# Optimization experiments

Hardware: AMD Instinct MI355X
Metric: run time of the kernel (lower is better)

The kernel has to match this reference:

```python
import jax, jax.numpy as jnp
from jax import lax
import numpy as np

B, T, H, K = 32, 512, 2048, 128


def setup_inputs() -> dict:
    key = jax.random.key(0)
    k1, k2, k3, k4, k5, k6, k7 = jax.random.split(key, 7)
    hiddens = jax.random.normal(k1, (B, T, H), dtype=jnp.float32)
    mask = jnp.ones((B, T), dtype=jnp.int32)  # mask[:,0] must be on (torchcrf)
    labels = jax.random.randint(k2, (B, T), 0, K)
    W = jax.random.normal(k3, (H, K), dtype=jnp.float32) * 0.02
    b = jnp.zeros((K,), dtype=jnp.float32)
    # torchcrf inits transitions uniform(-0.1, 0.1)
    start_transitions = jax.random.uniform(k4, (K,), minval=-0.1, maxval=0.1)
    end_transitions = jax.random.uniform(k5, (K,), minval=-0.1, maxval=0.1)
    transitions = jax.random.uniform(k6, (K, K), minval=-0.1, maxval=0.1)
    return {"hiddens": hiddens, "mask": mask, "labels": labels, "W": W, "b": b,
            "start_transitions": start_transitions, "end_transitions": end_transitions,
            "transitions": transitions}


def _crf_log_likelihood(emissions, tags, mask, start_t, end_t, trans):
    # emissions: [B,T,K], tags/mask: [B,T]
    Bn, Tn, Kn = emissions.shape
    maskf = mask.astype(emissions.dtype)
    # ---- numerator: score of the gold path ----
    score = start_t[tags[:, 0]] + emissions[jnp.arange(Bn), 0, tags[:, 0]]
    prev, cur = tags[:, :-1], tags[:, 1:]
    emit_cur = jnp.take_along_axis(emissions[:, 1:], cur[..., None], axis=-1)[..., 0]
    score = score + jnp.sum((trans[prev, cur] + emit_cur) * maskf[:, 1:], axis=1)
    last_idx = mask.sum(axis=1).astype(jnp.int32) - 1
    last_tags = jnp.take_along_axis(tags, last_idx[:, None], axis=1)[:, 0]
    score = score + end_t[last_tags]
    # ---- denominator: log partition via stable logsumexp scan ----
    def step(alpha, inp):
        emit_t, m_t = inp  # [B,K], [B]
        nxt = jax.nn.logsumexp(alpha[:, :, None] + trans[None] + emit_t[:, None, :], axis=1)
        alpha = jnp.where(m_t[:, None] > 0, nxt, alpha)
        return alpha, None
    alpha0 = start_t[None, :] + emissions[:, 0]
    emits = jnp.swapaxes(emissions[:, 1:], 0, 1)  # [T-1,B,K]
    ms = jnp.swapaxes(mask[:, 1:], 0, 1)          # [T-1,B]
    alpha, _ = lax.scan(step, alpha0, (emits, ms))
    logZ = jax.nn.logsumexp(alpha + end_t[None, :], axis=1)
    return score - logZ


def _viterbi_decode(emissions, mask, start_t, end_t, trans):
    Bn, Tn, Kn = emissions.shape
    tag_ids = jnp.arange(Kn, dtype=jnp.int32)
    def step(score, inp):
        emit_t, m_t = inp
        cand = score[:, :, None] + trans[None]          # [B,K,K] prev->cur
        bp = jnp.argmax(cand, axis=1).astype(jnp.int32)  # [B,K]
        best = jnp.max(cand, axis=1) + emit_t
        on = m_t[:, None] > 0
        new_score = jnp.where(on, best, score)
        bp = jnp.where(on, bp, tag_ids[None, :])  # identity for padded steps
        return new_score, bp
    score0 = start_t[None, :] + emissions[:, 0]
    emits = jnp.swapaxes(emissions[:, 1:], 0, 1)
    ms = jnp.swapaxes(mask[:, 1:], 0, 1)
    score, history = lax.scan(step, score0, (emits, ms))  # history: [T-1,B,K]
    last_tag = jnp.argmax(score + end_t[None, :], axis=1).astype(jnp.int32)  # [B]
    def back(tag, bp_t):
        tag = jnp.take_along_axis(bp_t, tag[:, None], axis=1)[:, 0]
        return tag, tag
    _, tags_prev = lax.scan(back, last_tag, history, reverse=True)  # [T-1,B]
    tags = jnp.concatenate([tags_prev, last_tag[None, :]], axis=0)  # [T,B]
    return jnp.swapaxes(tags, 0, 1)  # [B,T]


def reference(hiddens, mask, labels, W, b, start_transitions, end_transitions, transitions):
    logits = jnp.einsum('bth,hk->btk', hiddens, W) + b  # emission projection
    decode = _viterbi_decode(logits, mask, start_transitions, end_transitions, transitions)
    llh = _crf_log_likelihood(logits, labels, mask, start_transitions, end_transitions, transitions)
    loss = -jnp.mean(llh)  # -1 * crf(..., reduction='mean')
    return (decode, loss)
```

## Files before the change

### kernel.cpp

```cpp
#include <hip/hip_runtime.h>
#include <hip/hip_bf16.h>
#include <math.h>

#define BB 32
#define TT 512
#define HH 2048
#define KK 128

__global__ __launch_bounds__(512) void gemm_k(const float* __restrict__ hid,
                                              const float* __restrict__ Wm,
                                              const float* __restrict__ bias,
                                              float* __restrict__ logits,
                                              float* __restrict__ loss_slot) {
    __shared__ union {
        struct { float As[4][16][72]; float Bs[4][16][132]; } s;
        float4 red[16][128];
    } sm;
    const int tid = threadIdx.x, bid = blockIdx.x;
    if (bid == 0 && tid == 0) loss_slot[0] = 0.0f;
    const int g = tid >> 7, lt = tid & 127;
    const int rowBase = bid * 64;
    const int rowg = lt >> 4, colg = lt & 15;
    const int arow = lt >> 1, ahq = lt & 1;

    float acc[8][8];
#pragma unroll
    for (int i = 0; i < 8; i++)
#pragma unroll
        for (int j = 0; j < 8; j++) acc[i][j] = 0.0f;

    const float* hA = hid + (size_t)(rowBase + arow) * HH + g * 512 + ahq * 8;

    float4 a0, a1, bv[4];
    {
        const int h0 = g * 512;
        a0 = *(const float4*)(hA);
        a1 = *(const float4*)(hA + 4);
#pragma unroll
        for (int r = 0; r < 4; ++r) {
            int idx = r * 128 + lt;
// ... 47 lines not shown
        if (g == gp) {
#pragma unroll
            for (int i = 0; i < 8; ++i) {
                sm.red[i * 2][lt] = make_float4(acc[i][0], acc[i][1], acc[i][2], acc[i][3]);
                sm.red[i * 2 + 1][lt] = make_float4(acc[i][4], acc[i][5], acc[i][6], acc[i][7]);
            }
        }
        __syncthreads();
        if (g == 0) {
#pragma unroll
            for (int i = 0; i < 8; ++i) {
                float4 r0 = sm.red[i * 2][lt];
                float4 r1 = sm.red[i * 2 + 1][lt];
                acc[i][0] += r0.x; acc[i][1] += r0.y; acc[i][2] += r0.z; acc[i][3] += r0.w;
                acc[i][4] += r1.x; acc[i][5] += r1.y; acc[i][6] += r1.z; acc[i][7] += r1.w;
            }
        }
        __syncthreads();
    }
    if (g == 0) {
        float4 bb0 = *(const float4*)(bias + colg * 4);
        float4 bb1 = *(const float4*)(bias + 64 + colg * 4);
#pragma unroll
        for (int i = 0; i < 8; ++i) {
            int row = rowBase + rowg * 8 + i;
            *(float4*)(logits + (size_t)row * KK + colg * 4) =
                make_float4(acc[i][0] + bb0.x, acc[i][1] + bb0.y, acc[i][2] + bb0.z, acc[i][3] + bb0.w);
            *(float4*)(logits + (size_t)row * KK + 64 + colg * 4) =
                make_float4(acc[i][4] + bb1.x, acc[i][5] + bb1.y, acc[i][6] + bb1.z, acc[i][7] + bb1.w);
        }
    }
}

struct SMemB {
    float ubuf[2][144];
    float red[4];
    float vbuf[128];
};

__global__ __launch_bounds__(256) void scan_k(const float* __restrict__ logits,
                                              const int* __restrict__ mask,
                                              const int* __restrict__ labels,
                                              const float* __restrict__ startT,
                                              const float* __restrict__ endT,
                                              const float* __restrict__ trans,
                                              float* __restrict__ shist,
                                              float* __restrict__ out) {
    __shared__ SMemB sm;
    const int tid = threadIdx.x;
    const int bid = blockIdx.x;
    const float L2E = 1.4426950408889634f;
    const int s = tid & 3;
    const int jb = tid >> 2;
    const int j0 = jb * 2;
    const int padw = j0 + 4 * (j0 >> 5);
    const int lane = tid & 63;

    if (bid < BB) {
        const int b = bid;
        const float* lrow = logits + (size_t)b * TT * KK;
        unsigned long long mb[8];
#pragma unroll
        for (int c = 0; c < 8; ++c) mb[c] = __ballot(mask[b * TT + c * 64 + lane]);
        float V0[32], V1[32];
#pragma unroll
        for (int k = 0; k < 32; k++) {
            V0[k] = exp2f(trans[(s * 32 + k) * KK + j0] * L2E);
            V1[k] = exp2f(trans[(s * 32 + k) * KK + j0 + 1] * L2E);
        }
        float a0_ = (startT[j0] + lrow[j0]) * L2E;
        float a1_ = (startT[j0 + 1] + lrow[j0 + 1]) * L2E;
        float OFF = (startT[0] + lrow[0]) * L2E;
        float S0_ = exp2f(a0_ - OFF);
        float S1_ = exp2f(a1_ - OFF);
        if (s == 0) {
            sm.ubuf[0][padw] = S0_;
            sm.ubuf[0][padw + 1] = S1_;
        }
        float2 emq[4];
#pragma unroll
        for (int d = 0; d < 4; ++d) emq[d] = *(const float2*)(lrow + (size_t)(1 + d) * KK + j0);
        float2 scc = make_float2(exp2f(emq[0].x * L2E), exp2f(emq[0].y * L2E));
        __syncthreads();
        int cur = 0;
        for (int t = 1; t < TT; ++t) {
            float2 sc = scc;
            emq[0] = emq[1]; emq[1] = emq[2]; emq[2] = emq[3];
            if (t + 4 < TT) emq[3] = *(const float2*)(lrow + (size_t)(t + 4) * KK + j0);
            scc = make_float2(exp2f(emq[0].x * L2E), exp2f(emq[0].y * L2E));
            int mt = (int)((mb[t >> 6] >> (t & 63)) & 1ull);
            if (mt) {
                const float* ub = &sm.ubuf[cur][s * 36];
                float u00 = sm.ubuf[cur][0];
                float uu[32];
#pragma unroll
                for (int c = 0; c < 8; ++c) {
                    float4 v = *(const float4*)(ub + c * 4);
                    uu[c * 4] = v.x; uu[c * 4 + 1] = v.y; uu[c * 4 + 2] = v.z; uu[c * 4 + 3] = v.w;
                }
                float r00 = __builtin_amdgcn_rcpf(u00);
                OFF += log2f(u00);
                float p0[4] = {0.f, 0.f, 0.f, 0.f}, p1[4] = {0.f, 0.f, 0.f, 0.f};
#pragma unroll
                for (int k = 0; k < 32; k += 4) {
#pragma unroll
                    for (int q = 0; q < 4; ++q) {
                        p0[q] = fmaf(uu[k + q], V0[k + q], p0[q]);
                        p1[q] = fmaf(uu[k + q], V1[k + q], p1[q]);
                    }
                }
                float w0 = (p0[0] + p0[1]) + (p0[2] + p0[3]);
                float w1 = (p1[0] + p1[1]) + (p1[2] + p1[3]);
                w0 += __shfl_xor(w0, 1, 64);
                w0 += __shfl_xor(w0, 2, 64);
                w1 += __shfl_xor(w1, 1, 64);
                w1 += __shfl_xor(w1, 2, 64);
                S0_ = w0 * (sc.x * r00);
                S1_ = w1 * (sc.y * r00);
                if (s == 0) {
                    sm.ubuf[cur ^ 1][padw] = S0_;
                    sm.ubuf[cur ^ 1][padw + 1] = S1_;
                }
                cur ^= 1;
            }
            __syncthreads();
        }
        if (s == 0) {
            sm.vbuf[j0] = log2f(S0_) + endT[j0] * L2E;
            sm.vbuf[j0 + 1] = log2f(S1_) + endT[j0 + 1] * L2E;
        }
        __syncthreads();

        float part = 0.0f;
        for (int tt = tid; tt < TT; tt += 256) {
            if (tt == 0) {
                int l0 = labels[b * TT];
                part += startT[l0] + lrow[l0];
            } else if (mask[b * TT + tt]) {
                int lc = labels[b * TT + tt];
                int lp = labels[b * TT + tt - 1];
                part += trans[lp * KK + lc] + lrow[(size_t)tt * KK + lc];
            }
        }
#pragma unroll
        for (int d = 1; d < 64; d <<= 1) part += __shfl_xor(part, d, 64);
        int wid = tid >> 6;
        if (lane == 0) sm.red[wid] = part;
        __syncthreads();
        if (tid < 64) {
            float v0 = sm.vbuf[tid], v1 = sm.vbuf[tid + 64];
            float mx = fmaxf(v0, v1);
#pragma unroll
            for (int d = 1; d < 64; d <<= 1) mx = fmaxf(mx, __shfl_xor(mx, d, 64));
            float p = exp2f(v0 - mx) + exp2f(v1 - mx);
#pragma unroll
            for (int d = 1; d < 64; d <<= 1) p += __shfl_xor(p, d, 64);
            if (tid == 0) {
                int total = 0;
#pragma unroll
                for (int c = 0; c < 8; ++c) total += __popcll(mb[c]);
                float score = sm.red[0] + sm.red[1] + sm.red[2] + sm.red[3];
                score += endT[labels[b * TT + total - 1]];
                float logZ = (OFF + mx + log2f(p)) * 0.6931471805599453f;
                float llh = score - logZ;
                atomicAdd(out + BB * TT, -llh * (1.0f / 32.0f));
            }
        }
    } else {
        const int b = bid - BB;
        const float* lrow = logits + (size_t)b * TT * KK;
        float* hist = shist + (size_t)b * TT * KK;
        unsigned long long mb[8];
#pragma unroll
        for (int c = 0; c < 8; ++c) mb[c] = __ballot(mask[b * TT + c * 64 + lane]);
        float T0[32], T1[32];
#pragma unroll
        for (int k = 0; k < 32; k++) {
            T0[k] = trans[(s * 32 + k) * KK + j0];
            T1[k] = trans[(s * 32 + k) * KK + j0 + 1];
        }
        float s0_ = startT[j0] + lrow[j0];
        float s1_ = startT[j0 + 1] + lrow[j0 + 1];
        if (s == 0) {
            sm.ubuf[0][padw] = s0_;
            sm.ubuf[0][padw + 1] = s1_;
        } else if (s == 1) {
            *(float2*)(hist + j0) = make_float2(s0_, s1_);
        }
        float2 emq[4];
#pragma unroll
        for (int d = 0; d < 4; ++d) emq[d] = *(const float2*)(lrow + (size_t)(1 + d) * KK + j0);
        __syncthreads();
        int cur = 0;
        for (int t = 1; t < TT; ++t) {
            float2 em = emq[0];
            emq[0] = emq[1]; emq[1] = emq[2]; emq[2] = emq[3];
            if (t + 4 < TT) emq[3] = *(const float2*)(lrow + (size_t)(t + 4) * KK + j0);
            int mt = (int)((mb[t >> 6] >> (t & 63)) & 1ull);
            if (mt) {
                const float* ub = &sm.ubuf[cur][s * 36];
                float uu[32];
#pragma unroll
                for (int c = 0; c < 8; ++c) {
                    float4 v = *(const float4*)(ub + c * 4);
                    uu[c * 4] = v.x; uu[c * 4 + 1] = v.y; uu[c * 4 + 2] = v.z; uu[c * 4 + 3] = v.w;
                }
                float m0a = -3.0e38f, m0b = -3.0e38f, m1a = -3.0e38f, m1b = -3.0e38f;
#pragma unroll
                for (int k = 0; k < 32; k += 4) {
                    m0a = fmaxf(m0a, fmaxf(uu[k] + T0[k], uu[k + 1] + T0[k + 1]));
                    m0b = fmaxf(m0b, fmaxf(uu[k + 2] + T0[k + 2], uu[k + 3] + T0[k + 3]));
                    m1a = fmaxf(m1a, fmaxf(uu[k] + T1[k], uu[k + 1] + T1[k + 1]));
                    m1b = fmaxf(m1b, fmaxf(uu[k + 2] + T1[k + 2], uu[k + 3] + T1[k + 3]));
                }
                float m0 = fmaxf(m0a, m0b), m1 = fmaxf(m1a, m1b);
                m0 = fmaxf(m0, __shfl_xor(m0, 1, 64));
                m0 = fmaxf(m0, __shfl_xor(m0, 2, 64));
                m1 = fmaxf(m1, __shfl_xor(m1, 1, 64));
                m1 = fmaxf(m1, __shfl_xor(m1, 2, 64));
                s0_ = m0 + em.x;
                s1_ = m1 + em.y;
                if (s == 0) {
                    sm.ubuf[cur ^ 1][padw] = s0_;
                    sm.ubuf[cur ^ 1][padw + 1] = s1_;
                } else if (s == 1) {
                    *(float2*)(hist + (size_t)t * KK + j0) = make_float2(s0_, s1_);
                }
                cur ^= 1;
            } else {
                if (s == 1) *(float2*)(hist + (size_t)t * KK + j0) = make_float2(s0_, s1_);
            }
            __syncthreads();
        }
    }
}

__global__ __launch_bounds__(256) void bp_k(const float* __restrict__ shist,
                                            const float* __restrict__ trans,
                                            const int* __restrict__ mask,
                                            unsigned char* __restrict__ bp) {
    const int t = blockIdx.x + 1;
    const int tid = threadIdx.x;
    const int j = tid & 127, bg = tid >> 7;
    __shared__ float sc[BB][KK];
#pragma unroll
    for (int r = 0; r < 4; ++r) {
        int f = tid + r * 256;
        int bb2 = f >> 5, c4 = (f & 31) * 4;
        *(float4*)&sc[bb2][c4] = *(const float4*)&shist[(size_t)bb2 * TT * KK + (size_t)(t - 1) * KK + c4];
    }
    __syncthreads();
    float m[16];
    int idx[16];
#pragma unroll
    for (int c = 0; c < 16; c++) { m[c] = -3.0e38f; idx[c] = 0; }
    for (int i4 = 0; i4 < 32; ++i4) {
        const int ib = i4 * 4;
        float tr0 = trans[(ib + 0) * KK + j];
        float tr1 = trans[(ib + 1) * KK + j];
        float tr2 = trans[(ib + 2) * KK + j];
        float tr3 = trans[(ib + 3) * KK + j];
#pragma unroll
        for (int c = 0; c < 16; c++) {
            float4 s4 = *(const float4*)&sc[bg + 2 * c][ib];
            float c0 = s4.x + tr0, c1 = s4.y + tr1, c2 = s4.z + tr2, c3 = s4.w + tr3;
// ... 50 lines not shown
                int t_row = ph * 64 + 1 + r;
                if (t_row < TT) {
                    unsigned int vv = (unsigned int)__shfl((int)reg[r], tag >> 1, 64);
                    tag = (int)((vv >> ((tag & 1) * 8)) & 0xffu);
                    if (lane == 0) tagbuf[t_row - 1] = tag;
                }
            }
            if (lane == 0) handoff = tag;
        }
        __syncthreads();
    }
    out[b * TT + tid] = (float)tagbuf[tid];
}

extern "C" void kernel_launch(void* const* d_in, const int* in_sizes, int n_in,
                              void* d_out, int out_size, void* d_ws, size_t ws_size,
                              hipStream_t stream) {
    const float* hid = (const float*)d_in[0];
    const int* mask = (const int*)d_in[1];
    const int* labels = (const int*)d_in[2];
    const float* Wm = (const float*)d_in[3];
    const float* bias = (const float*)d_in[4];
    const float* startT = (const float*)d_in[5];
    const float* endT = (const float*)d_in[6];
    const float* trans = (const float*)d_in[7];
    float* out = (float*)d_out;
    char* ws = (char*)d_ws;

    float* logits = (float*)ws;
    float* shist = (float*)(ws + 8388608);
    unsigned char* bp = (unsigned char*)(ws + 16777216);

    gemm_k<<<256, 512, 0, stream>>>(hid, Wm, bias, logits, out + BB * TT);
    scan_k<<<64, 256, 0, stream>>>(logits, mask, labels, startT, endT, trans, shist, out);
    bp_k<<<TT - 1, 256, 0, stream>>>(shist, trans, mask, bp);
    bt_k<<<BB, 512, 0, stream>>>(shist, endT, bp, out);
}
```

Measured before the change: 665.4 us.

## Stage emission logits in shared-memory chunks and batch Viterbi history stores

Both sequential scan loops now load emissions in chunks of 8 timesteps. Each thread issues one coalesced float4 load per chunk, and the data is double-buffered in LDS instead of each thread keeping a 4-deep register queue of strided float2 global loads. The Viterbi path also buffers its per-step score history in registers and writes all 8 steps to global memory at the end of each chunk, rather than storing every step. The aim is to take global-load latency and store traffic off the per-timestep critical path. The cost is more LDS, extra register pressure, and moving the exp2 of the emission back onto the serial dependency chain in the forward scan.

```diff
diff --git a/kernel.cpp b/kernel.cpp
--- a/kernel.cpp
+++ b/kernel.cpp
@@ -6,6 +6,7 @@
 #define TT 512
 #define HH 2048
 #define KK 128
+#define CH 8
 
 __global__ __launch_bounds__(512) void gemm_k(const float* __restrict__ hid,
                                               const float* __restrict__ Wm,
@@ -121,6 +122,7 @@
 
 struct SMemB {
     float ubuf[2][144];
+    float em[2][CH * KK];
     float red[4];
     float vbuf[128];
 };
@@ -142,6 +144,7 @@
     const int j0 = jb * 2;
     const int padw = j0 + 4 * (j0 >> 5);
     const int lane = tid & 63;
+    const int NCHUNK = TT / CH;
 
     if (bid < BB) {
         const int b = bid;
@@ -164,53 +167,61 @@
             sm.ubuf[0][padw] = S0_;
             sm.ubuf[0][padw + 1] = S1_;
         }
-        float2 emq[4];
-#pragma unroll
-        for (int d = 0; d < 4; ++d) emq[d] = *(const float2*)(lrow + (size_t)(1 + d) * KK + j0);
-        float2 scc = make_float2(exp2f(emq[0].x * L2E), exp2f(emq[0].y * L2E));
+        float4 st = *(const float4*)(lrow + tid * 4);
+        *(float4*)&sm.em[0][tid * 4] = st;
         __syncthreads();
         int cur = 0;
-        for (int t = 1; t < TT; ++t) {
-            float2 sc = scc;
-            emq[0] = emq[1]; emq[1] = emq[2]; emq[2] = emq[3];
-            if (t + 4 < TT) emq[3] = *(const float2*)(lrow + (size_t)(t + 4) * KK + j0);
-            scc = make_float2(exp2f(emq[0].x * L2E), exp2f(emq[0].y * L2E));
-            int mt = (int)((mb[t >> 6] >> (t & 63)) & 1ull);
-            if (mt) {
-                const float* ub = &sm.ubuf[cur][s * 36];
-                float u00 = sm.ubuf[cur][0];
-                float uu[32];
-#pragma unroll
-                for (int c = 0; c < 8; ++c) {
-                    float4 v = *(const float4*)(ub + c * 4);
-                    uu[c * 4] = v.x; uu[c * 4 + 1] = v.y; uu[c * 4 + 2] = v.z; uu[c * 4 + 3] = v.w;
-                }
-                float r00 = __builtin_amdgcn_rcpf(u00);
-                OFF += log2f(u00);
-                float p0[4] = {0.f, 0.f, 0.f, 0.f}, p1[4] = {0.f, 0.f, 0.f, 0.f};
-#pragma unroll
-                for (int k = 0; k < 32; k += 4) {
-#pragma unroll
-                    for (int q = 0; q < 4; ++q) {
-                        p0[q] = fmaf(uu[k + q], V0[k + q], p0[q]);
-                        p1[q] = fmaf(uu[k + q], V1[k + q], p1[q]);
+        for (int c = 0; c < NCHUNK; ++c) {
+            const int buf = c & 1;
+#pragma unroll
+            for (int r = 0; r < CH; ++r) {
+                const int t = c * CH + r;
+                if (r == 0 && c + 1 < NCHUNK)
+                    st = *(const float4*)(lrow + (size_t)(c + 1) * CH * KK + tid * 4);
+                if (t > 0) {
+                    int mt = (int)((mb[t >> 6] >> (t & 63)) & 1ull);
+                    if (mt) {
+                        float2 em = *(const float2*)&sm.em[buf][r * KK + j0];
+                        const float* ub = &sm.ubuf[cur][s * 36];
+                        float u00 = sm.ubuf[cur][0];
+                        float uu[32];
+#pragma unroll
+                        for (int cc = 0; cc < 8; ++cc) {
+                            float4 v = *(const float4*)(ub + cc * 4);
+                            uu[cc * 4] = v.x; uu[cc * 4 + 1] = v.y; uu[cc * 4 + 2] = v.z; uu[cc * 4 + 3] = v.w;
+                        }
+                        float r00 = __builtin_amdgcn_rcpf(u00);
+                        OFF += log2f(u00);
+                        float sc0 = exp2f(em.x * L2E) * r00;
+                        float sc1 = exp2f(em.y * L2E) * r00;
+                        float p0[4] = {0.f, 0.f, 0.f, 0.f}, p1[4] = {0.f, 0.f, 0.f, 0.f};
+#pragma unroll
+                        for (int k = 0; k < 32; k += 4) {
+#pragma unroll
+                            for (int q = 0; q < 4; ++q) {
+                                p0[q] = fmaf(uu[k + q], V0[k + q], p0[q]);
+                                p1[q] = fmaf(uu[k + q], V1[k + q], p1[q]);
+                            }
+                        }
+                        float w0 = (p0[0] + p0[1]) + (p0[2] + p0[3]);
+                        float w1 = (p1[0] + p1[1]) + (p1[2] + p1[3]);
+                        w0 += __shfl_xor(w0, 1, 64);
+                        w0 += __shfl_xor(w0, 2, 64);
+                        w1 += __shfl_xor(w1, 1, 64);
+                        w1 += __shfl_xor(w1, 2, 64);
+                        S0_ = w0 * sc0;
+                        S1_ = w1 * sc1;
+                        if (s == 0) {
+                            sm.ubuf[cur ^ 1][padw] = S0_;
+                            sm.ubuf[cur ^ 1][padw + 1] = S1_;
+                        }
+                        cur ^= 1;
                     }
                 }
-                float w0 = (p0[0] + p0[1]) + (p0[2] + p0[3]);
-                float w1 = (p1[0] + p1[1]) + (p1[2] + p1[3]);
-                w0 += __shfl_xor(w0, 1, 64);
-                w0 += __shfl_xor(w0, 2, 64);
-                w1 += __shfl_xor(w1, 1, 64);
-                w1 += __shfl_xor(w1, 2, 64);
-                S0_ = w0 * (sc.x * r00);
-                S1_ = w1 * (sc.y * r00);
-                if (s == 0) {
-                    sm.ubuf[cur ^ 1][padw] = S0_;
-                    sm.ubuf[cur ^ 1][padw + 1] = S1_;
-                }
-                cur ^= 1;
-            }
-            __syncthreads();
+                if (r == CH - 1 && c + 1 < NCHUNK)
+                    *(float4*)&sm.em[buf ^ 1][tid * 4] = st;
+                __syncthreads();
+            }
         }
         if (s == 0) {
             sm.vbuf[j0] = log2f(S0_) + endT[j0] * L2E;
@@ -271,53 +282,62 @@
         if (s == 0) {
             sm.ubuf[0][padw] = s0_;
             sm.ubuf[0][padw + 1] = s1_;
-        } else if (s == 1) {
-            *(float2*)(hist + j0) = make_float2(s0_, s1_);
-        }
-        float2 emq[4];
-#pragma unroll
-        for (int d = 0; d < 4; ++d) emq[d] = *(const float2*)(lrow + (size_t)(1 + d) * KK + j0);
+        }
+        float4 st = *(const float4*)(lrow + tid * 4);
+        *(float4*)&sm.em[0][tid * 4] = st;
         __syncthreads();
         int cur = 0;
-        for (int t = 1; t < TT; ++t) {
-            float2 em = emq[0];
-            emq[0] = emq[1]; emq[1] = emq[2]; emq[2] = emq[3];
-            if (t + 4 < TT) emq[3] = *(const float2*)(lrow + (size_t)(t + 4) * KK + j0);
-            int mt = (int)((mb[t >> 6] >> (t & 63)) & 1ull);
-            if (mt) {
-                const float* ub = &sm.ubuf[cur][s * 36];
-                float uu[32];
-#pragma unroll
-                for (int c = 0; c < 8; ++c) {
-                    float4 v = *(const float4*)(ub + c * 4);
-                    uu[c * 4] = v.x; uu[c * 4 + 1] = v.y; uu[c * 4 + 2] = v.z; uu[c * 4 + 3] = v.w;
+        float2 hb[CH];
+        for (int c = 0; c < NCHUNK; ++c) {
+            const int buf = c & 1;
+#pragma unroll
+            for (int r = 0; r < CH; ++r) {
+                const int t = c * CH + r;
+                if (r == 0 && c + 1 < NCHUNK)
+                    st = *(const float4*)(lrow + (size_t)(c + 1) * CH * KK + tid * 4);
+                if (t > 0) {
+                    int mt = (int)((mb[t >> 6] >> (t & 63)) & 1ull);
+                    if (mt) {
+                        float2 em = *(const float2*)&sm.em[buf][r * KK + j0];
+                        const float* ub = &sm.ubuf[cur][s * 36];
+                        float uu[32];
+#pragma unroll
+                        for (int cc = 0; cc < 8; ++cc) {
+                            float4 v = *(const float4*)(ub + cc * 4);
+                            uu[cc * 4] = v.x; uu[cc * 4 + 1] = v.y; uu[cc * 4 + 2] = v.z; uu[cc * 4 + 3] = v.w;
+                        }
+                        float m0a = -3.0e38f, m0b = -3.0e38f, m1a = -3.0e38f, m1b = -3.0e38f;
+#pragma unroll
+                        for (int k = 0; k < 32; k += 4) {
+                            m0a = fmaxf(m0a, fmaxf(uu[k] + T0[k], uu[k + 1] + T0[k + 1]));
+                            m0b = fmaxf(m0b, fmaxf(uu[k + 2] + T0[k + 2], uu[k + 3] + T0[k + 3]));
+                            m1a = fmaxf(m1a, fmaxf(uu[k] + T1[k], uu[k + 1] + T1[k + 1]));
+                            m1b = fmaxf(m1b, fmaxf(uu[k + 2] + T1[k + 2], uu[k + 3] + T1[k + 3]));
+                        }
+                        float m0 = fmaxf(m0a, m0b), m1 = fmaxf(m1a, m1b);
+                        m0 = fmaxf(m0, __shfl_xor(m0, 1, 64));
+                        m0 = fmaxf(m0, __shfl_xor(m0, 2, 64));
+                        m1 = fmaxf(m1, __shfl_xor(m1, 1, 64));
+                        m1 = fmaxf(m1, __shfl_xor(m1, 2, 64));
+                        s0_ = m0 + em.x;
+                        s1_ = m1 + em.y;
+                        if (s == 0) {
+                            sm.ubuf[cur ^ 1][padw] = s0_;
+                            sm.ubuf[cur ^ 1][padw + 1] = s1_;
+                        }
+                        cur ^= 1;
+                    }
                 }
-                float m0a = -3.0e38f, m0b = -3.0e38f, m1a = -3.0e38f, m1b = -3.0e38f;
-#pragma unroll
-                for (int k = 0; k < 32; k += 4) {
-                    m0a = fmaxf(m0a, fmaxf(uu[k] + T0[k], uu[k + 1] + T0[k + 1]));
-                    m0b = fmaxf(m0b, fmaxf(uu[k + 2] + T0[k + 2], uu[k + 3] + T0[k + 3]));
-                    m1a = fmaxf(m1a, fmaxf(uu[k] + T1[k], uu[k + 1] + T1[k + 1]));
-                    m1b = fmaxf(m1b, fmaxf(uu[k + 2] + T1[k + 2], uu[k + 3] + T1[k + 3]));
-                }
-                float m0 = fmaxf(m0a, m0b), m1 = fmaxf(m1a, m1b);
-                m0 = fmaxf(m0, __shfl_xor(m0, 1, 64));
-                m0 = fmaxf(m0, __shfl_xor(m0, 2, 64));
-                m1 = fmaxf(m1, __shfl_xor(m1, 1, 64));
-                m1 = fmaxf(m1, __shfl_xor(m1, 2, 64));
-                s0_ = m0 + em.x;
-                s1_ = m1 + em.y;
-                if (s == 0) {
-                    sm.ubuf[cur ^ 1][padw] = s0_;
-                    sm.ubuf[cur ^ 1][padw + 1] = s1_;
-                } else if (s == 1) {
-                    *(float2*)(hist + (size_t)t * KK + j0) = make_float2(s0_, s1_);
-                }
-                cur ^= 1;
-            } else {
-                if (s == 1) *(float2*)(hist + (size_t)t * KK + j0) = make_float2(s0_, s1_);
-            }
-            __syncthreads();
+                hb[r] = make_float2(s0_, s1_);
+                if (r == CH - 1 && c + 1 < NCHUNK)
+                    *(float4*)&sm.em[buf ^ 1][tid * 4] = st;
+                __syncthreads();
+            }
+            if (s == 1) {
+#pragma unroll
+                for (int r = 0; r < CH; ++r)
+                    *(float2*)(hist + (size_t)(c * CH + r) * KK + j0) = hb[r];
+            }
         }
     }
 }
```

New measurement: 657.2 us. No clear change (-1.2%).

## Run CRF forward and Viterbi scans in a single wavefront without block barriers

Applied to the files above, without the earlier changes.

The sequential scan kernel moves from 256 threads per batch row to one 64-lane wavefront. Each lane owns four tags and half of the previous-tag range, and a single cross-half shuffle replaces the 4-way shuffle reduction. This removes the per-timestep __syncthreads and the shared double buffer, since one wavefront can rely on in-order LDS visibility. Emissions are now prefetched in 8-step chunks. In exchange each lane does four times more FMAs or max operations per step and holds 128 transition values in registers, which raises register pressure and per-step serial work.

```diff
diff --git a/kernel.cpp b/kernel.cpp
--- a/kernel.cpp
+++ b/kernel.cpp
@@ -119,107 +119,114 @@
     }
 }
 
-struct SMemB {
-    float ubuf[2][144];
-    float red[4];
-    float vbuf[128];
-};
-
-__global__ __launch_bounds__(256) void scan_k(const float* __restrict__ logits,
-                                              const int* __restrict__ mask,
-                                              const int* __restrict__ labels,
-                                              const float* __restrict__ startT,
-                                              const float* __restrict__ endT,
-                                              const float* __restrict__ trans,
-                                              float* __restrict__ shist,
-                                              float* __restrict__ out) {
-    __shared__ SMemB sm;
-    const int tid = threadIdx.x;
+__global__ __launch_bounds__(64, 1) void scan_k(const float* __restrict__ logits,
+                                                const int* __restrict__ mask,
+                                                const int* __restrict__ labels,
+                                                const float* __restrict__ startT,
+                                                const float* __restrict__ endT,
+                                                const float* __restrict__ trans,
+                                                float* __restrict__ shist,
+                                                float* __restrict__ out) {
+    __shared__ float sal[128];
+    const int lane = threadIdx.x;
     const int bid = blockIdx.x;
     const float L2E = 1.4426950408889634f;
-    const int s = tid & 3;
-    const int jb = tid >> 2;
-    const int j0 = jb * 2;
-    const int padw = j0 + 4 * (j0 >> 5);
-    const int lane = tid & 63;
+    const int q = lane & 31;
+    const int h = lane >> 5;
+    const int j0 = 4 * q;
 
     if (bid < BB) {
         const int b = bid;
         const float* lrow = logits + (size_t)b * TT * KK;
         unsigned long long mb[8];
 #pragma unroll
-        for (int c = 0; c < 8; ++c) mb[c] = __ballot(mask[b * TT + c * 64 + lane]);
-        float V0[32], V1[32];
-#pragma unroll
-        for (int k = 0; k < 32; k++) {
-            V0[k] = exp2f(trans[(s * 32 + k) * KK + j0] * L2E);
-            V1[k] = exp2f(trans[(s * 32 + k) * KK + j0 + 1] * L2E);
-        }
-        float a0_ = (startT[j0] + lrow[j0]) * L2E;
-        float a1_ = (startT[j0 + 1] + lrow[j0 + 1]) * L2E;
+        for (int c = 0; c < 8; ++c) mb[c] = __ballot(mask[b * TT + c * 64 + lane] != 0);
+
+        float2 Vp0[32], Vp1[32], Vp2[32], Vp3[32];
+#pragma unroll
+        for (int p = 0; p < 32; ++p) {
+            float4 ra = *(const float4*)&trans[(size_t)(h * 64 + 2 * p) * KK + j0];
+            float4 rb = *(const float4*)&trans[(size_t)(h * 64 + 2 * p + 1) * KK + j0];
+            Vp0[p] = make_float2(exp2f(ra.x * L2E), exp2f(rb.x * L2E));
+            Vp1[p] = make_float2(exp2f(ra.y * L2E), exp2f(rb.y * L2E));
+            Vp2[p] = make_float2(exp2f(ra.z * L2E), exp2f(rb.z * L2E));
+            Vp3[p] = make_float2(exp2f(ra.w * L2E), exp2f(rb.w * L2E));
+        }
+        float4 st4 = *(const float4*)(startT + j0);
+        float4 e0 = *(const float4*)(lrow + j0);
         float OFF = (startT[0] + lrow[0]) * L2E;
-        float S0_ = exp2f(a0_ - OFF);
-        float S1_ = exp2f(a1_ - OFF);
-        if (s == 0) {
-            sm.ubuf[0][padw] = S0_;
-            sm.ubuf[0][padw + 1] = S1_;
-        }
-        float2 emq[4];
-#pragma unroll
-        for (int d = 0; d < 4; ++d) emq[d] = *(const float2*)(lrow + (size_t)(1 + d) * KK + j0);
-        float2 scc = make_float2(exp2f(emq[0].x * L2E), exp2f(emq[0].y * L2E));
-        __syncthreads();
-        int cur = 0;
-        for (int t = 1; t < TT; ++t) {
-            float2 sc = scc;
-            emq[0] = emq[1]; emq[1] = emq[2]; emq[2] = emq[3];
-            if (t + 4 < TT) emq[3] = *(const float2*)(lrow + (size_t)(t + 4) * KK + j0);
-            scc = make_float2(exp2f(emq[0].x * L2E), exp2f(emq[0].y * L2E));
-            int mt = (int)((mb[t >> 6] >> (t & 63)) & 1ull);
-            if (mt) {
-                const float* ub = &sm.ubuf[cur][s * 36];
-                float u00 = sm.ubuf[cur][0];
-                float uu[32];
-#pragma unroll
-                for (int c = 0; c < 8; ++c) {
-                    float4 v = *(const float4*)(ub + c * 4);
-                    uu[c * 4] = v.x; uu[c * 4 + 1] = v.y; uu[c * 4 + 2] = v.z; uu[c * 4 + 3] = v.w;
+        float S0 = exp2f((st4.x + e0.x) * L2E - OFF);
+        float S1 = exp2f((st4.y + e0.y) * L2E - OFF);
+        float S2 = exp2f((st4.z + e0.z) * L2E - OFF);
+        float S3 = exp2f((st4.w + e0.w) * L2E - OFF);
+        float s0bc = 1.0f;
+        if (h == 0) *(float4*)&sal[j0] = make_float4(S0, S1, S2, S3);
+
+        float4 emc[8], emn[8];
+#pragma unroll
+        for (int d = 0; d < 8; ++d) emc[d] = *(const float4*)(lrow + (size_t)d * KK + j0);
+
+        for (int c = 0; c < 64; ++c) {
+            if (c < 63) {
+#pragma unroll
+                for (int d = 0; d < 8; ++d)
+                    emn[d] = *(const float4*)(lrow + (size_t)((c + 1) * 8 + d) * KK + j0);
+            }
+#pragma unroll
+            for (int r = 0; r < 8; ++r) {
+                const int t = c * 8 + r;
+                if (t > 0 && ((mb[t >> 6] >> (t & 63)) & 1ull)) {
+                    float rinv = __builtin_amdgcn_rcpf(s0bc);
+                    OFF += log2f(s0bc);
+                    float2 a0 = make_float2(0.f, 0.f), a1 = make_float2(0.f, 0.f);
+                    float2 a2 = make_float2(0.f, 0.f), a3 = make_float2(0.f, 0.f);
+                    const float* base = &sal[h * 64];
+#pragma unroll
+                    for (int i = 0; i < 16; ++i) {
+                        float4 U = *(const float4*)(base + 4 * i);
+                        a0.x = fmaf(U.x, Vp0[2 * i].x, a0.x);     a0.y = fmaf(U.y, Vp0[2 * i].y, a0.y);
+                        a1.x = fmaf(U.x, Vp1[2 * i].x, a1.x);     a1.y = fmaf(U.y, Vp1[2 * i].y, a1.y);
+                        a2.x = fmaf(U.x, Vp2[2 * i].x, a2.x);     a2.y = fmaf(U.y, Vp2[2 * i].y, a2.y);
+                        a3.x = fmaf(U.x, Vp3[2 * i].x, a3.x);     a3.y = fmaf(U.y, Vp3[2 * i].y, a3.y);
+                        a0.x = fmaf(U.z, Vp0[2 * i + 1].x, a0.x); a0.y = fmaf(U.w, Vp0[2 * i + 1].y, a0.y);
+                        a1.x = fmaf(U.z, Vp1[2 * i + 1].x, a1.x); a1.y = fmaf(U.w, Vp1[2 * i + 1].y, a1.y);
+                        a2.x = fmaf(U.z, Vp2[2 * i + 1].x, a2.x); a2.y = fmaf(U.w, Vp2[2 * i + 1].y, a2.y);
+                        a3.x = fmaf(U.z, Vp3[2 * i + 1].x, a3.x); a3.y = fmaf(U.w, Vp3[2 * i + 1].y, a3.y);
+                    }
+                    float w0 = a0.x + a0.y, w1 = a1.x + a1.y;
+                    float w2 = a2.x + a2.y, w3 = a3.x + a3.y;
+                    float x0 = __shfl_xor(w0, 32, 64), x1 = __shfl_xor(w1, 32, 64);
+                    float x2 = __shfl_xor(w2, 32, 64), x3 = __shfl_xor(w3, 32, 64);
+                    w0 += x0; w1 += x1; w2 += x2; w3 += x3;
+                    float4 e = emc[r];
+                    S0 = w0 * (exp2f(e.x * L2E) * rinv);
+                    S1 = w1 * (exp2f(e.y * L2E) * rinv);
+                    S2 = w2 * (exp2f(e.z * L2E) * rinv);
+                    S3 = w3 * (exp2f(e.w * L2E) * rinv);
+                    s0bc = __shfl(S0, 0, 64);
+                    if (h == 0) *(float4*)&sal[j0] = make_float4(S0, S1, S2, S3);
                 }
-                float r00 = __builtin_amdgcn_rcpf(u00);
-                OFF += log2f(u00);
-                float p0[4] = {0.f, 0.f, 0.f, 0.f}, p1[4] = {0.f, 0.f, 0.f, 0.f};
-#pragma unroll
-                for (int k = 0; k < 32; k += 4) {
-#pragma unroll
-                    for (int q = 0; q < 4; ++q) {
-                        p0[q] = fmaf(uu[k + q], V0[k + q], p0[q]);
-                        p1[q] = fmaf(uu[k + q], V1[k + q], p1[q]);
-                    }
-                }
-                float w0 = (p0[0] + p0[1]) + (p0[2] + p0[3]);
-                float w1 = (p1[0] + p1[1]) + (p1[2] + p1[3]);
-                w0 += __shfl_xor(w0, 1, 64);
-                w0 += __shfl_xor(w0, 2, 64);
-                w1 += __shfl_xor(w1, 1, 64);
-                w1 += __shfl_xor(w1, 2, 64);
-                S0_ = w0 * (sc.x * r00);
-                S1_ = w1 * (sc.y * r00);
-                if (s == 0) {
-                    sm.ubuf[cur ^ 1][padw] = S0_;
-                    sm.ubuf[cur ^ 1][padw + 1] = S1_;
-                }
-                cur ^= 1;
-            }
-            __syncthreads();
-        }
-        if (s == 0) {
-            sm.vbuf[j0] = log2f(S0_) + endT[j0] * L2E;
-            sm.vbuf[j0 + 1] = log2f(S1_) + endT[j0 + 1] * L2E;
-        }
-        __syncthreads();
+            }
+#pragma unroll
+            for (int d = 0; d < 8; ++d) emc[d] = emn[d];
+        }
+
+        float4 et = *(const float4*)(endT + j0);
+        float v0 = log2f(S0) + et.x * L2E;
+        float v1 = log2f(S1) + et.y * L2E;
+        float v2 = log2f(S2) + et.z * L2E;
+        float v3 = log2f(S3) + et.w * L2E;
+        float mx = fmaxf(fmaxf(v0, v1), fmaxf(v2, v3));
+#pragma unroll
+        for (int d = 1; d < 64; d <<= 1) mx = fmaxf(mx, __shfl_xor(mx, d, 64));
+        float p = (h == 0) ? (exp2f(v0 - mx) + exp2f(v1 - mx) + exp2f(v2 - mx) + exp2f(v3 - mx)) : 0.0f;
+#pragma unroll
+        for (int d = 1; d < 64; d <<= 1) p += __shfl_xor(p, d, 64);
 
         float part = 0.0f;
-        for (int tt = tid; tt < TT; tt += 256) {
+#pragma unroll
+        for (int it = 0; it < 8; ++it) {
+            int tt = lane + it * 64;
             if (tt == 0) {
                 int l0 = labels[b * TT];
                 part += startT[l0] + lrow[l0];
@@ -231,27 +238,15 @@
         }
 #pragma unroll
         for (int d = 1; d < 64; d <<= 1) part += __shfl_xor(part, d, 64);
-        int wid = tid >> 6;
-        if (lane == 0) sm.red[wid] = part;
-        __syncthreads();
-        if (tid < 64) {
-            float v0 = sm.vbuf[tid], v1 = sm.vbuf[tid + 64];
-            float mx = fmaxf(v0, v1);
-#pragma unroll
-            for (int d = 1; d < 64; d <<= 1) mx = fmaxf(mx, __shfl_xor(mx, d, 64));
-            float p = exp2f(v0 - mx) + exp2f(v1 - mx);
-#pragma unroll
-            for (int d = 1; d < 64; d <<= 1) p += __shfl_xor(p, d, 64);
-            if (tid == 0) {
-                int total = 0;
-#pragma unroll
-                for (int c = 0; c < 8; ++c) total += __popcll(mb[c]);
-                float score = sm.red[0] + sm.red[1] + sm.red[2] + sm.red[3];
-                score += endT[labels[b * TT + total - 1]];
-                float logZ = (OFF + mx + log2f(p)) * 0.6931471805599453f;
-                float llh = score - logZ;
-                atomicAdd(out + BB * TT, -llh * (1.0f / 32.0f));
-            }
+
+        if (lane == 0) {
+            int total = 0;
+#pragma unroll
+            for (int c = 0; c < 8; ++c) total += __popcll(mb[c]);
+            float score = part + endT[labels[b * TT + total - 1]];
+            float logZ = (OFF + mx + log2f(p)) * 0.6931471805599453f;
+            float llh = score - logZ;
+            atomicAdd(out + BB * TT, -llh * (1.0f / 32.0f));
         }
     } else {
         const int b = bid - BB;
@@ -259,65 +254,76 @@
         float* hist = shist + (size_t)b * TT * KK;
         unsigned long long mb[8];
 #pragma unroll
-        for (int c = 0; c < 8; ++c) mb[c] = __ballot(mask[b * TT + c * 64 + lane]);
-        float T0[32], T1[32];
-#pragma unroll
-        for (int k = 0; k < 32; k++) {
-            T0[k] = trans[(s * 32 + k) * KK + j0];
-            T1[k] = trans[(s * 32 + k) * KK + j0 + 1];
-        }
-        float s0_ = startT[j0] + lrow[j0];
-        float s1_ = startT[j0 + 1] + lrow[j0 + 1];
-        if (s == 0) {
-            sm.ubuf[0][padw] = s0_;
-            sm.ubuf[0][padw + 1] = s1_;
-        } else if (s == 1) {
-            *(float2*)(hist + j0) = make_float2(s0_, s1_);
-        }
-        float2 emq[4];
-#pragma unroll
-        for (int d = 0; d < 4; ++d) emq[d] = *(const float2*)(lrow + (size_t)(1 + d) * KK + j0);
-        __syncthreads();
-        int cur = 0;
-        for (int t = 1; t < TT; ++t) {
-            float2 em = emq[0];
-            emq[0] = emq[1]; emq[1] = emq[2]; emq[2] = emq[3];
-            if (t + 4 < TT) emq[3] = *(const float2*)(lrow + (size_t)(t + 4) * KK + j0);
-            int mt = (int)((mb[t >> 6] >> (t & 63)) & 1ull);
-            if (mt) {
-                const float* ub = &sm.ubuf[cur][s * 36];
-                float uu[32];
-#pragma unroll
-                for (int c = 0; c < 8; ++c) {
-                    float4 v = *(const float4*)(ub + c * 4);
-                    uu[c * 4] = v.x; uu[c * 4 + 1] = v.y; uu[c * 4 + 2] = v.z; uu[c * 4 + 3] = v.w;
+        for (int c = 0; c < 8; ++c) mb[c] = __ballot(mask[b * TT + c * 64 + lane] != 0);
+
+        float2 Tp0[32], Tp1[32], Tp2[32], Tp3[32];
+#pragma unroll
+        for (int p = 0; p < 32; ++p) {
+            float4 ra = *(const float4*)&trans[(size_t)(h * 64 + 2 * p) * KK + j0];
+            float4 rb = *(const float4*)&trans[(size_t)(h * 64 + 2 * p + 1) * KK + j0];
+            Tp0[p] = make_float2(ra.x, rb.x);
+            Tp1[p] = make_float2(ra.y, rb.y);
+            Tp2[p] = make_float2(ra.z, rb.z);
+            Tp3[p] = make_float2(ra.w, rb.w);
+        }
+        float4 st4 = *(const float4*)(startT + j0);
+        float4 e0 = *(const float4*)(lrow + j0);
+        float S0 = st4.x + e0.x, S1 = st4.y + e0.y, S2 = st4.z + e0.z, S3 = st4.w + e0.w;
+        if (h == 0) {
+            *(float4*)&sal[j0] = make_float4(S0, S1, S2, S3);
+            *(float4*)(hist + j0) = make_float4(S0, S1, S2, S3);
+        }
+        float4 emc[8], emn[8];
+#pragma unroll
+        for (int d = 0; d < 8; ++d) emc[d] = *(const float4*)(lrow + (size_t)d * KK + j0);
+
+        for (int c = 0; c < 64; ++c) {
+            if (c < 63) {
+#pragma unroll
+                for (int d = 0; d < 8; ++d)
+                    emn[d] = *(const float4*)(lrow + (size_t)((c + 1) * 8 + d) * KK + j0);
+            }
+#pragma unroll
+            for (int r = 0; r < 8; ++r) {
+                const int t = c * 8 + r;
+                if (t > 0) {
+                    if ((mb[t >> 6] >> (t & 63)) & 1ull) {
+                        float m0 = -3.0e38f, m1 = -3.0e38f, m2 = -3.0e38f, m3 = -3.0e38f;
+                        const float* base = &sal[h * 64];
+#pragma unroll
+                        for (int i = 0; i < 16; ++i) {
+                            float4 U = *(const float4*)(base + 4 * i);
+                            float2 cA0 = make_float2(U.x + Tp0[2 * i].x, U.y + Tp0[2 * i].y);
+                            float2 cA1 = make_float2(U.x + Tp1[2 * i].x, U.y + Tp1[2 * i].y);
+                            float2 cA2 = make_float2(U.x + Tp2[2 * i].x, U.y + Tp2[2 * i].y);
+                            float2 cA3 = make_float2(U.x + Tp3[2 * i].x, U.y + Tp3[2 * i].y);
+                            m0 = fmaxf(m0, fmaxf(cA0.x, cA0.y));
+                            m1 = fmaxf(m1, fmaxf(cA1.x, cA1.y));
+                            m2 = fmaxf(m2, fmaxf(cA2.x, cA2.y));
+                            m3 = fmaxf(m3, fmaxf(cA3.x, cA3.y));
+                            float2 cB0 = make_float2(U.z + Tp0[2 * i + 1].x, U.w + Tp0[2 * i + 1].y);
+                            float2 cB1 = make_float2(U.z + Tp1[2 * i + 1].x, U.w + Tp1[2 * i + 1].y);
+                            float2 cB2 = make_float2(U.z + Tp2[2 * i + 1].x, U.w + Tp2[2 * i + 1].y);
+                            float2 cB3 = make_float2(U.z + Tp3[2 * i + 1].x, U.w + Tp3[2 * i + 1].y);
+                            m0 = fmaxf(m0, fmaxf(cB0.x, cB0.y));
+                            m1 = fmaxf(m1, fmaxf(cB1.x, cB1.y));
+                            m2 = fmaxf(m2, fmaxf(cB2.x, cB2.y));
+                            m3 = fmaxf(m3, fmaxf(cB3.x, cB3.y));
+                        }
+                        float x0 = __shfl_xor(m0, 32, 64), x1 = __shfl_xor(m1, 32, 64);
+                        float x2 = __shfl_xor(m2, 32, 64), x3 = __shfl_xor(m3, 32, 64);
+                        m0 = fmaxf(m0, x0); m1 = fmaxf(m1, x1);
+                        m2 = fmaxf(m2, x2); m3 = fmaxf(m3, x3);
+                        float4 e = emc[r];
+                        S0 = m0 + e.x; S1 = m1 + e.y; S2 = m2 + e.z; S3 = m3 + e.w;
+                        if (h == 0) *(float4*)&sal[j0] = make_float4(S0, S1, S2, S3);
+                    }
+                    if (h == 0)
+                        *(float4*)(hist + (size_t)t * KK + j0) = make_float4(S0, S1, S2, S3);
                 }
-                float m0a = -3.0e38f, m0b = -3.0e38f, m1a = -3.0e38f, m1b = -3.0e38f;
-#pragma unroll
-                for (int k = 0; k < 32; k += 4) {
-                    m0a = fmaxf(m0a, fmaxf(uu[k] + T0[k], uu[k + 1] + T0[k + 1]));
-                    m0b = fmaxf(m0b, fmaxf(uu[k + 2] + T0[k + 2], uu[k + 3] + T0[k + 3]));
-                    m1a = fmaxf(m1a, fmaxf(uu[k] + T1[k], uu[k + 1] + T1[k + 1]));
-                    m1b = fmaxf(m1b, fmaxf(uu[k + 2] + T1[k + 2], uu[k + 3] + T1[k + 3]));
-                }
-                float m0 = fmaxf(m0a, m0b), m1 = fmaxf(m1a, m1b);
-                m0 = fmaxf(m0, __shfl_xor(m0, 1, 64));
-                m0 = fmaxf(m0, __shfl_xor(m0, 2, 64));
-                m1 = fmaxf(m1, __shfl_xor(m1, 1, 64));
-                m1 = fmaxf(m1, __shfl_xor(m1, 2, 64));
-                s0_ = m0 + em.x;
-                s1_ = m1 + em.y;
-                if (s == 0) {
-                    sm.ubuf[cur ^ 1][padw] = s0_;
-                    sm.ubuf[cur ^ 1][padw + 1] = s1_;
-                } else if (s == 1) {
-                    *(float2*)(hist + (size_t)t * KK + j0) = make_float2(s0_, s1_);
-                }
-                cur ^= 1;
-            } else {
-                if (s == 1) *(float2*)(hist + (size_t)t * KK + j0) = make_float2(s0_, s1_);
-            }
-            __syncthreads();
+            }
+#pragma unroll
+            for (int d = 0; d < 8; ++d) emc[d] = emn[d];
         }
     }
 }
@@ -434,7 +440,7 @@
     unsigned char* bp = (unsigned char*)(ws + 16777216);
 
     gemm_k<<<256, 512, 0, stream>>>(hid, Wm, bias, logits, out + BB * TT);
-    scan_k<<<64, 256, 0, stream>>>(logits, mask, labels, startT, endT, trans, shist, out);
+    scan_k<<<64, 64, 0, stream>>>(logits, mask, labels, startT, endT, trans, shist, out);
     bp_k<<<TT - 1, 256, 0, stream>>>(shist, trans, mask, bp);
     bt_k<<<BB, 512, 0, stream>>>(shist, endT, bp, out);
 }
```

Result: slower. 1.086 ms (+63.3%).

## Restructure CRF scan to one thread per tag with full transition column in registers

Applied to the files above, without the earlier changes.

The forward and Viterbi scans now use 128 threads per block, one per target tag. Each thread holds the full 128-entry transition column in registers, which removes the 4-way split and the cross-lane shuffle reductions on every step. Emissions are prefetched in chunks of 16 timesteps, and history writes are batched per chunk. The per-step barrier now runs only on masked steps. The trade-off is a 128-term serial FMA or max chain per step instead of 32 terms, plus high register pressure from holding 128 floats of the column.

```diff
diff --git a/kernel.cpp b/kernel.cpp
--- a/kernel.cpp
+++ b/kernel.cpp
@@ -6,6 +6,7 @@
 #define TT 512
 #define HH 2048
 #define KK 128
+#define CH 16
 
 __global__ __launch_bounds__(512) void gemm_k(const float* __restrict__ hid,
                                               const float* __restrict__ Wm,
@@ -120,106 +121,97 @@
 }
 
 struct SMemB {
-    float ubuf[2][144];
+    float sal[2][KK];
     float red[4];
-    float vbuf[128];
 };
 
-__global__ __launch_bounds__(256) void scan_k(const float* __restrict__ logits,
-                                              const int* __restrict__ mask,
-                                              const int* __restrict__ labels,
-                                              const float* __restrict__ startT,
-                                              const float* __restrict__ endT,
-                                              const float* __restrict__ trans,
-                                              float* __restrict__ shist,
-                                              float* __restrict__ out) {
+__global__ __launch_bounds__(128, 1) void scan_k(const float* __restrict__ logits,
+                                                 const int* __restrict__ mask,
+                                                 const int* __restrict__ labels,
+                                                 const float* __restrict__ startT,
+                                                 const float* __restrict__ endT,
+                                                 const float* __restrict__ trans,
+                                                 float* __restrict__ shist,
+                                                 float* __restrict__ out) {
     __shared__ SMemB sm;
     const int tid = threadIdx.x;
     const int bid = blockIdx.x;
+    const int lane = tid & 63, wv = tid >> 6;
     const float L2E = 1.4426950408889634f;
-    const int s = tid & 3;
-    const int jb = tid >> 2;
-    const int j0 = jb * 2;
-    const int padw = j0 + 4 * (j0 >> 5);
-    const int lane = tid & 63;
+    const int j = tid;
 
     if (bid < BB) {
         const int b = bid;
         const float* lrow = logits + (size_t)b * TT * KK;
         unsigned long long mb[8];
 #pragma unroll
-        for (int c = 0; c < 8; ++c) mb[c] = __ballot(mask[b * TT + c * 64 + lane]);
-        float V0[32], V1[32];
-#pragma unroll
-        for (int k = 0; k < 32; k++) {
-            V0[k] = exp2f(trans[(s * 32 + k) * KK + j0] * L2E);
-            V1[k] = exp2f(trans[(s * 32 + k) * KK + j0 + 1] * L2E);
-        }
-        float a0_ = (startT[j0] + lrow[j0]) * L2E;
-        float a1_ = (startT[j0 + 1] + lrow[j0 + 1]) * L2E;
+        for (int c = 0; c < 8; ++c) mb[c] = __ballot(mask[b * TT + c * 64 + lane] != 0);
+
+        float V[128];
+#pragma unroll
+        for (int k = 0; k < 128; ++k) V[k] = exp2f(trans[(size_t)k * KK + j] * L2E);
+
         float OFF = (startT[0] + lrow[0]) * L2E;
-        float S0_ = exp2f(a0_ - OFF);
-        float S1_ = exp2f(a1_ - OFF);
-        if (s == 0) {
-            sm.ubuf[0][padw] = S0_;
-            sm.ubuf[0][padw + 1] = S1_;
-        }
-        float2 emq[4];
-#pragma unroll
-        for (int d = 0; d < 4; ++d) emq[d] = *(const float2*)(lrow + (size_t)(1 + d) * KK + j0);
-        float2 scc = make_float2(exp2f(emq[0].x * L2E), exp2f(emq[0].y * L2E));
-        __syncthreads();
+        float S = exp2f((startT[j] + lrow[j]) * L2E - OFF);
+        sm.sal[0][j] = S;
         int cur = 0;
-        for (int t = 1; t < TT; ++t) {
-            float2 sc = scc;
-            emq[0] = emq[1]; emq[1] = emq[2]; emq[2] = emq[3];
-            if (t + 4 < TT) emq[3] = *(const float2*)(lrow + (size_t)(t + 4) * KK + j0);
-            scc = make_float2(exp2f(emq[0].x * L2E), exp2f(emq[0].y * L2E));
-            int mt = (int)((mb[t >> 6] >> (t & 63)) & 1ull);
-            if (mt) {
-                const float* ub = &sm.ubuf[cur][s * 36];
-                float u00 = sm.ubuf[cur][0];
-                float uu[32];
-#pragma unroll
-                for (int c = 0; c < 8; ++c) {
-                    float4 v = *(const float4*)(ub + c * 4);
-                    uu[c * 4] = v.x; uu[c * 4 + 1] = v.y; uu[c * 4 + 2] = v.z; uu[c * 4 + 3] = v.w;
+
+        float emc[CH], emn[CH];
+#pragma unroll
+        for (int d = 0; d < CH; ++d) emc[d] = lrow[(size_t)d * KK + j];
+        __syncthreads();
+
+        for (int c = 0; c < TT / CH; ++c) {
+            if (c + 1 < TT / CH) {
+#pragma unroll
+                for (int d = 0; d < CH; ++d)
+                    emn[d] = lrow[(size_t)((c + 1) * CH + d) * KK + j];
+            }
+#pragma unroll
+            for (int r = 0; r < CH; ++r) {
+                const int t = c * CH + r;
+                if (t > 0 && ((mb[t >> 6] >> (t & 63)) & 1ull)) {
+                    const float4* base = (const float4*)sm.sal[cur];
+                    float a0 = 0.f, a1 = 0.f, a2 = 0.f, a3 = 0.f;
+                    float u0;
+#pragma unroll
+                    for (int i = 0; i < 32; ++i) {
+                        float4 U = base[i];
+                        if (i == 0) u0 = U.x;
+                        a0 = fmaf(U.x, V[4 * i + 0], a0);
+                        a1 = fmaf(U.y, V[4 * i + 1], a1);
+                        a2 = fmaf(U.z, V[4 * i + 2], a2);
+                        a3 = fmaf(U.w, V[4 * i + 3], a3);
+                    }
+                    float rinv = __builtin_amdgcn_rcpf(u0);
+                    OFF += log2f(u0);
+                    float w = (a0 + a1) + (a2 + a3);
+                    S = w * (exp2f(emc[r] * L2E) * rinv);
+                    sm.sal[cur ^ 1][j] = S;
+                    cur ^= 1;
+                    __syncthreads();
                 }
-                float r00 = __builtin_amdgcn_rcpf(u00);
-                OFF += log2f(u00);
-                float p0[4] = {0.f, 0.f, 0.f, 0.f}, p1[4] = {0.f, 0.f, 0.f, 0.f};
-#pragma unroll
-                for (int k = 0; k < 32; k += 4) {
-#pragma unroll
-                    for (int q = 0; q < 4; ++q) {
-                        p0[q] = fmaf(uu[k + q], V0[k + q], p0[q]);
-                        p1[q] = fmaf(uu[k + q], V1[k + q], p1[q]);
-                    }
-                }
-                float w0 = (p0[0] + p0[1]) + (p0[2] + p0[3]);
-                float w1 = (p1[0] + p1[1]) + (p1[2] + p1[3]);
-                w0 += __shfl_xor(w0, 1, 64);
-                w0 += __shfl_xor(w0, 2, 64);
-                w1 += __shfl_xor(w1, 1, 64);
-                w1 += __shfl_xor(w1, 2, 64);
-                S0_ = w0 * (sc.x * r00);
-                S1_ = w1 * (sc.y * r00);
-                if (s == 0) {
-                    sm.ubuf[cur ^ 1][padw] = S0_;
-                    sm.ubuf[cur ^ 1][padw + 1] = S1_;
-                }
-                cur ^= 1;
-            }
-            __syncthreads();
-        }
-        if (s == 0) {
-            sm.vbuf[j0] = log2f(S0_) + endT[j0] * L2E;
-            sm.vbuf[j0 + 1] = log2f(S1_) + endT[j0 + 1] * L2E;
-        }
-        __syncthreads();
+            }
+#pragma unroll
+            for (int d = 0; d < CH; ++d) emc[d] = emn[d];
+        }
+
+        float v = log2f(S) + endT[j] * L2E;
+        float mx = v;
+#pragma unroll
+        for (int d = 1; d < 64; d <<= 1) mx = fmaxf(mx, __shfl_xor(mx, d, 64));
+        if (lane == 0) sm.red[wv] = mx;
+        __syncthreads();
+        mx = fmaxf(sm.red[0], sm.red[1]);
+        float p = exp2f(v - mx);
+#pragma unroll
+        for (int d = 1; d < 64; d <<= 1) p += __shfl_xor(p, d, 64);
+        if (lane == 0) sm.red[2 + wv] = p;
 
         float part = 0.0f;
-        for (int tt = tid; tt < TT; tt += 256) {
+#pragma unroll
+        for (int it = 0; it < 4; ++it) {
+            int tt = tid + it * 128;
             if (tt == 0) {
                 int l0 = labels[b * TT];
                 part += startT[l0] + lrow[l0];
@@ -231,27 +223,18 @@
         }
 #pragma unroll
         for (int d = 1; d < 64; d <<= 1) part += __shfl_xor(part, d, 64);
-        int wid = tid >> 6;
-        if (lane == 0) sm.red[wid] = part;
-        __syncthreads();
-        if (tid < 64) {
-            float v0 = sm.vbuf[tid], v1 = sm.vbuf[tid + 64];
-            float mx = fmaxf(v0, v1);
-#pragma unroll
-            for (int d = 1; d < 64; d <<= 1) mx = fmaxf(mx, __shfl_xor(mx, d, 64));
-            float p = exp2f(v0 - mx) + exp2f(v1 - mx);
-#pragma unroll
-            for (int d = 1; d < 64; d <<= 1) p += __shfl_xor(p, d, 64);
-            if (tid == 0) {
-                int total = 0;
-#pragma unroll
-                for (int c = 0; c < 8; ++c) total += __popcll(mb[c]);
-                float score = sm.red[0] + sm.red[1] + sm.red[2] + sm.red[3];
-                score += endT[labels[b * TT + total - 1]];
-                float logZ = (OFF + mx + log2f(p)) * 0.6931471805599453f;
-                float llh = score - logZ;
-                atomicAdd(out + BB * TT, -llh * (1.0f / 32.0f));
-            }
+        __syncthreads();
+        if (lane == 0) sm.red[wv] = part;
+        __syncthreads();
+        if (tid == 0) {
+            int total = 0;
+#pragma unroll
+            for (int c = 0; c < 8; ++c) total += __popcll(mb[c]);
+            float score = sm.red[0] + sm.red[1] + endT[labels[b * TT + total - 1]];
+            float pp = sm.red[2] + sm.red[3];
+            float logZ = (OFF + mx + log2f(pp)) * 0.6931471805599453f;
+            float llh = score - logZ;
+            atomicAdd(out + BB * TT, -llh * (1.0f / 32.0f));
         }
     } else {
         const int b = bid - BB;
@@ -259,65 +242,56 @@
         float* hist = shist + (size_t)b * TT * KK;
         unsigned long long mb[8];
 #pragma unroll
-        for (int c = 0; c < 8; ++c) mb[c] = __ballot(mask[b * TT + c * 64 + lane]);
-        float T0[32], T1[32];
-#pragma unroll
-        for (int k = 0; k < 32; k++) {
-            T0[k] = trans[(s * 32 + k) * KK + j0];
-            T1[k] = trans[(s * 32 + k) * KK + j0 + 1];
-        }
-        float s0_ = startT[j0] + lrow[j0];
-        float s1_ = startT[j0 + 1] + lrow[j0 + 1];
-        if (s == 0) {
-            sm.ubuf[0][padw] = s0_;
-            sm.ubuf[0][padw + 1] = s1_;
-        } else if (s == 1) {
-            *(float2*)(hist + j0) = make_float2(s0_, s1_);
-        }
-        float2 emq[4];
-#pragma unroll
-        for (int d = 0; d < 4; ++d) emq[d] = *(const float2*)(lrow + (size_t)(1 + d) * KK + j0);
-        __syncthreads();
+        for (int c = 0; c < 8; ++c) mb[c] = __ballot(mask[b * TT + c * 64 + lane] != 0);
+
+        float T[128];
+#pragma unroll
+        for (int k = 0; k < 128; ++k) T[k] = trans[(size_t)k * KK + j];
+
+        float S = startT[j] + lrow[j];
+        sm.sal[0][j] = S;
         int cur = 0;
-        for (int t = 1; t < TT; ++t) {
-            float2 em = emq[0];
-            emq[0] = emq[1]; emq[1] = emq[2]; emq[2] = emq[3];
-            if (t + 4 < TT) emq[3] = *(const float2*)(lrow + (size_t)(t + 4) * KK + j0);
-            int mt = (int)((mb[t >> 6] >> (t & 63)) & 1ull);
-            if (mt) {
-                const float* ub = &sm.ubuf[cur][s * 36];
-                float uu[32];
-#pragma unroll
-                for (int c = 0; c < 8; ++c) {
-                    float4 v = *(const float4*)(ub + c * 4);
-                    uu[c * 4] = v.x; uu[c * 4 + 1] = v.y; uu[c * 4 + 2] = v.z; uu[c * 4 + 3] = v.w;
+
+        float emc[CH], emn[CH], hb[CH];
+#pragma unroll
+        for (int d = 0; d < CH; ++d) emc[d] = lrow[(size_t)d * KK + j];
+        __syncthreads();
+
+        for (int c = 0; c < TT / CH; ++c) {
+            if (c + 1 < TT / CH) {
+#pragma unroll
+                for (int d = 0; d < CH; ++d)
+                    emn[d] = lrow[(size_t)((c + 1) * CH + d) * KK + j];
+            }
+#pragma unroll
+            for (int r = 0; r < CH; ++r) {
+                const int t = c * CH + r;
+                if (t > 0 && ((mb[t >> 6] >> (t & 63)) & 1ull)) {
+                    const float4* base = (const float4*)sm.sal[cur];
+                    float m0 = -3.0e38f, m1 = -3.0e38f, m2 = -3.0e38f, m3 = -3.0e38f;
+#pragma unroll
+                    for (int i = 0; i < 32; ++i) {
+                        float4 U = base[i];
+                        float c0 = U.x + T[4 * i + 0];
+                        float c1 = U.y + T[4 * i + 1];
+                        float c2 = U.z + T[4 * i + 2];
+                        float c3 = U.w + T[4 * i + 3];
+                        m0 = fmaxf(m0, fmaxf(c0, c1));
+                        m1 = fmaxf(m1, fmaxf(c2, c3));
+                    }
+                    m2 = fmaxf(m0, m1);
+                    S = m2 + emc[r];
+                    sm.sal[cur ^ 1][j] = S;
+                    cur ^= 1;
+                    __syncthreads();
                 }
-                float m0a = -3.0e38f, m0b = -3.0e38f, m1a = -3.0e38f, m1b = -3.0e38f;
-#pragma unroll
-                for (int k = 0; k < 32; k += 4) {
-                    m0a = fmaxf(m0a, fmaxf(uu[k] + T0[k], uu[k + 1] + T0[k + 1]));
-                    m0b = fmaxf(m0b, fmaxf(uu[k + 2] + T0[k + 2], uu[k + 3] + T0[k + 3]));
-                    m1a = fmaxf(m1a, fmaxf(uu[k] + T1[k], uu[k + 1] + T1[k + 1]));
-                    m1b = fmaxf(m1b, fmaxf(uu[k + 2] + T1[k + 2], uu[k + 3] + T1[k + 3]));
-                }
-                float m0 = fmaxf(m0a, m0b), m1 = fmaxf(m1a, m1b);
-                m0 = fmaxf(m0, __shfl_xor(m0, 1, 64));
-                m0 = fmaxf(m0, __shfl_xor(m0, 2, 64));
-                m1 = fmaxf(m1, __shfl_xor(m1, 1, 64));
-                m1 = fmaxf(m1, __shfl_xor(m1, 2, 64));
-                s0_ = m0 + em.x;
-                s1_ = m1 + em.y;
-                if (s == 0) {
-                    sm.ubuf[cur ^ 1][padw] = s0_;
-                    sm.ubuf[cur ^ 1][padw + 1] = s1_;
-                } else if (s == 1) {
-                    *(float2*)(hist + (size_t)t * KK + j0) = make_float2(s0_, s1_);
-                }
-                cur ^= 1;
-            } else {
-                if (s == 1) *(float2*)(hist + (size_t)t * KK + j0) = make_float2(s0_, s1_);
-            }
-            __syncthreads();
+                hb[r] = S;
+            }
+#pragma unroll
+            for (int r = 0; r < CH; ++r)
+                hist[(size_t)(c * CH + r) * KK + j] = hb[r];
+#pragma unroll
+            for (int d = 0; d < CH; ++d) emc[d] = emn[d];
         }
     }
 }
@@ -434,7 +408,7 @@
     unsigned char* bp = (unsigned char*)(ws + 16777216);
 
     gemm_k<<<256, 512, 0, stream>>>(hid, Wm, bias, logits, out + BB * TT);
-    scan_k<<<64, 256, 0, stream>>>(logits, mask, labels, startT, endT, trans, shist, out);
+    scan_k<<<64, 128, 0, stream>>>(logits, mask, labels, startT, endT, trans, shist, out);
     bp_k<<<TT - 1, 256, 0, stream>>>(shist, trans, mask, bp);
     bt_k<<<BB, 512, 0, stream>>>(shist, endT, bp, out);
 }
```

Result: slower. 849.0 us (+27.6%).
